# Kernel tuning notes

Hardware: AMD Instinct MI355X
Metric: run time of the kernel (lower is better)

Reference implementation:

```python
import jax, jax.numpy as jnp
import numpy as np

D_MODEL = 1024
N_HEADS = 16
HEAD_DIM = D_MODEL // N_HEADS


def setup_inputs() -> dict:
    key = jax.random.key(0)
    k1, k2, k3, k4, k5 = jax.random.split(key, 5)
    s = 0.02
    return {
        "x": jax.random.normal(k1, (2, 2048, D_MODEL), dtype=jnp.float32),
        "w_qkv": jax.random.normal(k2, (D_MODEL, 3 * D_MODEL), dtype=jnp.float32) * s,
        "b_qkv": jax.random.normal(k3, (3 * D_MODEL,), dtype=jnp.float32) * s,
        "w_proj": jax.random.normal(k4, (D_MODEL, D_MODEL), dtype=jnp.float32) * s,
        "b_proj": jax.random.normal(k5, (D_MODEL,), dtype=jnp.float32) * s,
    }


def reference(x, w_qkv, b_qkv, w_proj, b_proj):
    B, T, C = x.shape
    # fused qkv projection: [B,T,3C] -> [3,B,H,T,Dh]
    qkv = x @ w_qkv + b_qkv
    qkv = qkv.reshape(B, T, 3, N_HEADS, HEAD_DIM).transpose(2, 0, 3, 1, 4)
    q, k, v = qkv[0], qkv[1], qkv[2]
    scale = 1.0 / np.sqrt(HEAD_DIM).astype(np.float32)
    att = jnp.einsum("bhtd,bhsd->bhts", q, k) * scale  # [B,H,T,T]
    causal = jnp.triu(jnp.ones((T, T), dtype=bool), k=1)
    att = jnp.where(causal, -jnp.inf, att)
    att = jax.nn.softmax(att, axis=-1)
    # dropout is identity in eval / p=0
    out = jnp.einsum("bhts,bhsd->bhtd", att, v)  # [B,H,T,Dh]
    out = out.transpose(0, 2, 1, 3).reshape(B, T, C)
    return out @ w_proj + b_proj
```

## Files before the change

### kernel.cpp

```cpp
#include <hip/hip_runtime.h>
#include <hip/hip_bf16.h>
#include <stdint.h>

#define MROWS 4096
#define DMODEL 1024
#define NQKV 3072
#define TSEQ 2048

typedef __attribute__((ext_vector_type(8))) short short8;
typedef __attribute__((ext_vector_type(4))) short short4v;
typedef __attribute__((ext_vector_type(4))) float floatx4;
typedef unsigned short ushort_t;

#define TILE_ELEMS 4608
#define BH_TILE_STRIDE 147456

#define QSCALE 0.1803368801111204f

static __device__ __forceinline__ unsigned short f2bf(float f) {
    union { float f; unsigned u; } v; v.f = f;
    unsigned r = v.u + 0x7fff + ((v.u >> 16) & 1);
    return (unsigned short)(r >> 16);
}


static __device__ __forceinline__ floatx4 mfma16(short4v a, short4v b, floatx4 c) {
#if defined(__HIP_DEVICE_COMPILE__)
#if __has_builtin(__builtin_amdgcn_mfma_f32_16x16x16bf16_1k)
    return __builtin_amdgcn_mfma_f32_16x16x16bf16_1k(a, b, c, 0, 0, 0);
#else
#error "mfma 16x16x16 bf16 builtin unavailable on device"
#endif
#else
    return c;
#endif
}

static __device__ __forceinline__ unsigned pk2bf(float a, float b) {
    unsigned ua = __float_as_uint(a) + 0x8000u;
    unsigned ub = __float_as_uint(b) + 0x8000u;
#if defined(__HIP_DEVICE_COMPILE__) && __has_builtin(__builtin_amdgcn_perm)
    return __builtin_amdgcn_perm(ub, ua, 0x07060302u);
#else
    return (ua >> 16) | (ub & 0xFFFF0000u);
#endif
}

static __device__ __forceinline__ unsigned cvtpk(float a, float b) {
#if defined(__HIP_DEVICE_COMPILE__)
    unsigned r;
    asm("v_cvt_pk_bf16_f32 %0, %1, %2" : "=v"(r) : "v"(a), "v"(b));
    return r;
#else
    return pk2bf(a, b);
#endif
}

static __device__ __forceinline__ float exp2_fast(float x) {
#if defined(__HIP_DEVICE_COMPILE__) && __has_builtin(__builtin_amdgcn_exp2f)
    return __builtin_amdgcn_exp2f(x);
#else
    return exp2f(x);
#endif
}

static __device__ __forceinline__ void glds16(const void* g, void* l) {
    __builtin_amdgcn_global_load_lds(
        (const __attribute__((address_space(1))) void*)g,
        (__attribute__((address_space(3))) void*)l, 16, 0, 0);
}

__global__ void cast_f32_bf16(const float* __restrict__ in,
                              ushort_t* __restrict__ out, int n) {
    int i = (blockIdx.x * blockDim.x + threadIdx.x) * 4;
    if (i < n) {
        float4 f = *(const float4*)(in + i);
        ushort4 o;
        o.x = f2bf(f.x); o.y = f2bf(f.y); o.z = f2bf(f.z); o.w = f2bf(f.w);
        *(ushort4*)(out + i) = o;
    }
}

__global__ void transpose_cast(const float* __restrict__ in,
                               ushort_t* __restrict__ out, int R, int C) {
    __shared__ float tile[32][33];
    int c0 = blockIdx.x * 32, r0 = blockIdx.y * 32;
    int tx = threadIdx.x & 31, ty = threadIdx.x >> 5;
    for (int i = 0; i < 4; i++) {
        int r = ty + i * 8;
        tile[r][tx] = in[(size_t)(r0 + r) * C + c0 + tx];
    }
    __syncthreads();
    for (int i = 0; i < 4; i++) {
        int r = ty + i * 8;
        out[(size_t)(c0 + r) * R + r0 + tx] = f2bf(tile[tx][r]);
    }
}

__global__ void transpose_v(const ushort_t* __restrict__ in,
                            ushort_t* __restrict__ out) {
    __shared__ ushort_t T[64][72];
    int tile = blockIdx.x, bh = blockIdx.y;
    int tid = threadIdx.x;
    int row = tid >> 2, q4 = tid & 3;
    const ushort_t* ip = in + ((size_t)bh * TSEQ + tile * 64) * 64;
#pragma unroll
    for (int p = 0; p < 2; p++) {
        int c = q4 * 16 + p * 8;
        *(uint4*)(&T[row][c]) = *(const uint4*)(ip + (size_t)row * 64 + c);
    }
    __syncthreads();
    ushort_t* op = out + (size_t)bh * BH_TILE_STRIDE + (size_t)tile * TILE_ELEMS;
#pragma unroll
    for (int p = 0; p < 2; p++) {
        int cbase = q4 * 16 + p * 8;
        ushort_t tmp[8];
#pragma unroll
        for (int e = 0; e < 8; e++) {
            int cp = cbase + e;
            int Q = cp >> 4, SB = (cp >> 2) & 3, J = cp & 3;
            int s = SB * 16 + Q * 4 + J;
            tmp[e] = T[s][row];
        }
        *(uint4*)(op + (size_t)row * 72 + cbase) = *(uint4*)tmp;
    }
}

template <int EPI, int MFRAG, int PERXCD>
__global__ __launch_bounds__(256, 3)
void gemm_glds(const ushort_t* __restrict__ A,
               const ushort_t* __restrict__ Bt,
               const float* __restrict__ bias,
               void* __restrict__ out0, void* __restrict__ out1, void* __restrict__ out2,
               int M, int N, int K) {
    __shared__ ushort_t As[MFRAG * 32 * 32];
    __shared__ ushort_t Bs[128 * 32];
    int tid = threadIdx.x;
    int wave = tid >> 6, lane = tid & 63;
    int quad = lane >> 4, l16 = lane & 15;
    int id = blockIdx.x;
    int xcd = id & 7, sidx = id >> 3;
    int m_idx = xcd * PERXCD + (sidx & (PERXCD - 1));
    int n_idx = sidx / PERXCD;
    int m0 = m_idx * (MFRAG * 32), n0 = n_idx * 128;
    int wm = (wave & 1) * (MFRAG * 16), wn = (wave >> 1) * 64;

    const floatx4 zero = {0.f, 0.f, 0.f, 0.f};
    floatx4 acc[MFRAG][4];
#pragma unroll
    for (int i = 0; i < MFRAG; i++)
#pragma unroll
        for (int j = 0; j < 4; j++) acc[i][j] = zero;

    int srow = tid >> 2, sc = tid & 3;
    const ushort_t* ag = A  + (size_t)(m0 + srow) * K + sc * 8;
    const ushort_t* bg = Bt + (size_t)(n0 + srow) * K + sc * 8;
    ushort_t* asw = As + wave * 512;
    ushort_t* bsw = Bs + wave * 512;

    for (int k0 = 0; k0 < K; k0 += 32) {
        glds16(ag + k0, asw);
        if (MFRAG == 4) glds16(ag + (size_t)64 * K + k0, asw + 2048);
        glds16(bg + k0, bsw);
        glds16(bg + (size_t)64 * K + k0, bsw + 2048);
        __syncthreads();
        short8 af[MFRAG], bf[4];
#pragma unroll
        for (int i = 0; i < MFRAG; i++)
            af[i] = *(const short8*)(As + (wm + i * 16 + l16) * 32 + quad * 8);
#pragma unroll
        for (int j = 0; j < 4; j++)
            bf[j] = *(const short8*)(Bs + (wn + j * 16 + l16) * 32 + quad * 8);
#pragma unroll
        for (int i = 0; i < MFRAG; i++)
#pragma unroll
            for (int j = 0; j < 4; j++)
                acc[i][j] = __builtin_amdgcn_mfma_f32_16x16x32_bf16(
                    af[i], bf[j], acc[i][j], 0, 0, 0);
        __syncthreads();
    }

    int sec = n0 >> 10;
    ushort_t* dst = (ushort_t*)(sec == 0 ? out0 : (sec == 1 ? out1 : out2));
#pragma unroll
    for (int i = 0; i < MFRAG; i++) {
        int row = m0 + wm + i * 16 + quad * 4;
#pragma unroll
        for (int j = 0; j < 4; j++) {
            int col = n0 + wn + j * 16 + l16;
            float bvs = bias[col];
#pragma unroll
            for (int r = 0; r < 4; r++) {
                float v = acc[i][j][r] + bvs;
                int rowr = row + r;
                if (EPI == 0) {
                    ((float*)out0)[(size_t)rowr * N + col] = v;
                } else {
                    int b = rowr >> 11, t = rowr & 2047;
                    int within = col & 1023, h = within >> 6, d = within & 63;
                    size_t bh = (size_t)(b * 16 + h);
                    if (sec == 0)
                        dst[(bh * 2048 + t) * 64 + d] = f2bf(v * QSCALE);
                    else if (sec == 1)
                        dst[bh * BH_TILE_STRIDE + (size_t)(t >> 6) * TILE_ELEMS
                            + (size_t)(t & 63) * 72 + d] = f2bf(v);
                    else
                        dst[(bh * 2048 + t) * 64 + d] = f2bf(v);
                }
            }
        }
    }
}

__global__ __launch_bounds__(256, 4)
void attn_kernel(const ushort_t* __restrict__ Qb,
                 const ushort_t* __restrict__ Kt,
                 const ushort_t* __restrict__ Vt,
                 ushort_t* __restrict__ outb) {
    __shared__ ushort_t Ks[2][64 * 72];
    __shared__ ushort_t Vs[2][64 * 72];
    int tid = threadIdx.x;
    int wave = tid >> 6, lane = tid & 63;
    int quad = lane >> 4, l16 = lane & 15;
    int id = blockIdx.x;
    int g = id >> 3;
    int bh = (id & 7) * 4 + (g >> 5);
    int qt = 31 - (g & 31);
    int b = bh >> 4, h = bh & 15;
    const ushort_t* qh = Qb + (size_t)bh * TSEQ * 64;
    const ushort_t* kh = Kt + (size_t)bh * BH_TILE_STRIDE;
    const ushort_t* vh = Vt + (size_t)bh * BH_TILE_STRIDE;
    const floatx4 zero = {0.f, 0.f, 0.f, 0.f};
    const short4v ones = {(short)0x3F80, (short)0x3F80, (short)0x3F80, (short)0x3F80};
    int lo8 = lane * 8;

    int q0 = qt * 64;
    int nsteps = qt + 1;

    int qrow = q0 + wave * 16 + l16;
    short8 qf0 = *(const short8*)(qh + (size_t)qrow * 64 + quad * 8);
    short8 qf1 = *(const short8*)(qh + (size_t)qrow * 64 + 32 + quad * 8);

    floatx4 Oacc[4];
#pragma unroll
    for (int j = 0; j < 4; j++) Oacc[j] = zero;
    floatx4 lacc = zero;

#pragma unroll
    for (int c = 0; c < 3; c++) {
        int cc = wave + 4 * c;
        if (cc < 9) {
            glds16(kh + cc * 512 + lo8, &Ks[0][cc * 512]);
            glds16(vh + cc * 512 + lo8, &Vs[0][cc * 512]);
        }
    }

    for (int step = 0; step < nsteps; step++) {
        int cur = step & 1;
        __syncthreads();
        if (step + 1 < nsteps) {
            const ushort_t* kt = kh + (size_t)(step + 1) * TILE_ELEMS;
            const ushort_t* vt = vh + (size_t)(step + 1) * TILE_ELEMS;
#pragma unroll
            for (int c = 0; c < 3; c++) {
                int cc = wave + 4 * c;
                if (cc < 9) {
                    glds16(kt + cc * 512 + lo8, &Ks[cur ^ 1][cc * 512]);
                    glds16(vt + cc * 512 + lo8, &Vs[cur ^ 1][cc * 512]);
                }
            }
        }
        const ushort_t* ks = &Ks[cur][0];
        const ushort_t* vs = &Vs[cur][0];

        floatx4 S[4];
        __builtin_amdgcn_s_setprio(1);
#pragma unroll
        for (int sb = 0; sb < 4; sb++) {
            short8 kf0 = *(const short8*)(ks + (sb * 16 + l16) * 72 + quad * 8);
            short8 kf1 = *(const short8*)(ks + (sb * 16 + l16) * 72 + 32 + quad * 8);
            floatx4 s = zero;
            s = __builtin_amdgcn_mfma_f32_16x16x32_bf16(kf0, qf0, s, 0, 0, 0);
            s = __builtin_amdgcn_mfma_f32_16x16x32_bf16(kf1, qf1, s, 0, 0, 0);
            S[sb] = s;
        }
        __builtin_amdgcn_s_setprio(0);
        if (step == nsteps - 1) {
            int ql = wave * 16 + l16;
#pragma unroll
            for (int sb = 0; sb < 4; sb++)
#pragma unroll
                for (int r = 0; r < 4; r++)
                    if (sb * 16 + quad * 4 + r > ql) S[sb][r] = -1e30f;
        }
#pragma unroll
        for (int sb = 0; sb < 4; sb++)
#pragma unroll
            for (int r = 0; r < 4; r++)
                S[sb][r] = exp2_fast(S[sb][r]);

        short4v pf[4];
#pragma unroll
        for (int sb = 0; sb < 4; sb++) {
            union { unsigned u[2]; short4v v; } pk;
            pk.u[0] = cvtpk(S[sb][0], S[sb][1]);
            pk.u[1] = cvtpk(S[sb][2], S[sb][3]);
            pf[sb] = pk.v;
        }
        __builtin_amdgcn_s_setprio(1);
        lacc = mfma16(ones, pf[0], lacc);
        lacc = mfma16(ones, pf[1], lacc);
        lacc = mfma16(ones, pf[2], lacc);
        lacc = mfma16(ones, pf[3], lacc);
#pragma unroll
        for (int jd = 0; jd < 4; jd++) {
            const ushort_t* vrow = vs + (jd * 16 + l16) * 72 + quad * 16;
            short8 vA = *(const short8*)(vrow);
            short8 vB = *(const short8*)(vrow + 8);
            short4v v0 = __builtin_shufflevector(vA, vA, 0, 1, 2, 3);
            short4v v1 = __builtin_shufflevector(vA, vA, 4, 5, 6, 7);
            short4v v2 = __builtin_shufflevector(vB, vB, 0, 1, 2, 3);
            short4v v3 = __builtin_shufflevector(vB, vB, 4, 5, 6, 7);
            Oacc[jd] = mfma16(v0, pf[0], Oacc[jd]);
            Oacc[jd] = mfma16(v1, pf[1], Oacc[jd]);
            Oacc[jd] = mfma16(v2, pf[2], Oacc[jd]);
            Oacc[jd] = mfma16(v3, pf[3], Oacc[jd]);
        }
        __builtin_amdgcn_s_setprio(0);
    }
    {
        float rl = 1.0f / lacc[0];
        int row = b * TSEQ + q0 + wave * 16 + l16;
#pragma unroll
        for (int jd = 0; jd < 4; jd++) {
            int col = h * 64 + jd * 16 + quad * 4;
            ushort4 o;
            o.x = f2bf(Oacc[jd][0] * rl);
            o.y = f2bf(Oacc[jd][1] * rl);
            o.z = f2bf(Oacc[jd][2] * rl);
            o.w = f2bf(Oacc[jd][3] * rl);
            *(ushort4*)(outb + (size_t)row * DMODEL + col) = o;
        }
    }
}

extern "C" void kernel_launch(void* const* d_in, const int* in_sizes, int n_in,
                              void* d_out, int out_size, void* d_ws, size_t ws_size,
                              hipStream_t stream) {
    const float* x      = (const float*)d_in[0];
    const float* w_qkv  = (const float*)d_in[1];
    const float* b_qkv  = (const float*)d_in[2];
    const float* w_proj = (const float*)d_in[3];
    const float* b_proj = (const float*)d_in[4];
    float* out = (float*)d_out;
    char* ws = (char*)d_ws;

    ushort_t* xb     = (ushort_t*)(ws);
    ushort_t* Vt     = (ushort_t*)(ws);
    ushort_t* wqkvT  = (ushort_t*)(ws + 8388608);
    ushort_t* wprojT = (ushort_t*)(ws + 10485760);
    ushort_t* Qb     = (ushort_t*)(ws + 14680064);
    ushort_t* Kt     = (ushort_t*)(ws + 23068672);
    ushort_t* Vb     = (ushort_t*)(ws + 32505856);
    ushort_t* attnb  = Vb;

    cast_f32_bf16<<<4096, 256, 0, stream>>>(x, xb, MROWS * DMODEL);
    transpose_cast<<<dim3(NQKV / 32, DMODEL / 32), 256, 0, stream>>>(w_qkv, wqkvT, DMODEL, NQKV);

    gemm_glds<1, 4, 4><<<768, 256, 0, stream>>>(
        xb, wqkvT, b_qkv, Qb, Kt, Vb, MROWS, NQKV, DMODEL);

    transpose_v<<<dim3(32, 32), 256, 0, stream>>>(Vb, Vt);
    transpose_cast<<<dim3(DMODEL / 32, DMODEL / 32), 256, 0, stream>>>(w_proj, wprojT, DMODEL, DMODEL);

    attn_kernel<<<dim3(1024), 256, 0, stream>>>(Qb, Kt, Vt, attnb);

    gemm_glds<0, 2, 8><<<512, 256, 0, stream>>>(
        attnb, wprojT, b_proj, out, nullptr, nullptr, MROWS, DMODEL, DMODEL);
}
```

Measured before the change: 195.4 us.

## Balance causal attention work by splitting long query tiles across blocks

Replaces the one-block-per-query-tile attention kernel with a balanced split. Each block either pairs a short query tile with the first half of a long tile's KV range, or handles the second half of a long tile. For long tiles, unnormalized partial outputs and row sums go to fp32 workspace and are merged by a new combine kernel. A paired-tile fallback kernel, which takes the row sum from a shuffle reduction instead of an MFMA, is used when the workspace is too small. This trades an extra launch and fp32 partial traffic for even per-block work in place of the triangular imbalance.

```diff
diff --git a/kernel.cpp b/kernel.cpp
--- a/kernel.cpp
+++ b/kernel.cpp
@@ -213,7 +213,184 @@
 }
 
 __global__ __launch_bounds__(256, 4)
-void attn_kernel(const ushort_t* __restrict__ Qb,
+void attn_split(const ushort_t* __restrict__ Qb,
+                const ushort_t* __restrict__ Kt,
+                const ushort_t* __restrict__ Vt,
+                ushort_t* __restrict__ outb,
+                float* __restrict__ PO_a, float* __restrict__ PO_b,
+                float* __restrict__ Pl_a, float* __restrict__ Pl_b) {
+    __shared__ ushort_t Ks[2][64 * 72];
+    __shared__ ushort_t Vs[2][64 * 72];
+    int tid = threadIdx.x;
+    int wave = tid >> 6, lane = tid & 63;
+    int quad = lane >> 4, l16 = lane & 15;
+    int id = blockIdx.x;
+    int g = id >> 3;
+    int bh = (id & 7) * 4 + (g >> 5);
+    int rem = g & 31;
+    int p = rem >> 1, sub = rem & 1;
+    int b = bh >> 4, h = bh & 15;
+    const ushort_t* qh = Qb + (size_t)bh * TSEQ * 64;
+    const ushort_t* kh = Kt + (size_t)bh * BH_TILE_STRIDE;
+    const ushort_t* vh = Vt + (size_t)bh * BH_TILE_STRIDE;
+    const floatx4 zero = {0.f, 0.f, 0.f, 0.f};
+    const short4v ones = {(short)0x3F80, (short)0x3F80, (short)0x3F80, (short)0x3F80};
+    int lo8 = lane * 8;
+
+    int nseg = sub ? 1 : 2;
+    for (int seg = 0; seg < nseg; seg++) {
+        int qt, k0, cnt, mode;
+        if (sub)           { qt = 31 - p; k0 = 16 - p; cnt = 16;     mode = 2; }
+        else if (seg == 0) { qt = p;      k0 = 0;      cnt = p + 1;  mode = 0; }
+        else               { qt = 31 - p; k0 = 0;      cnt = 16 - p; mode = 1; }
+
+        int qrow = qt * 64 + wave * 16 + l16;
+        short8 qf0 = *(const short8*)(qh + (size_t)qrow * 64 + quad * 8);
+        short8 qf1 = *(const short8*)(qh + (size_t)qrow * 64 + 32 + quad * 8);
+
+        floatx4 Oacc[4];
+#pragma unroll
+        for (int j = 0; j < 4; j++) Oacc[j] = zero;
+        floatx4 lacc = zero;
+
+        __syncthreads();
+        {
+            const ushort_t* kt0 = kh + (size_t)k0 * TILE_ELEMS;
+            const ushort_t* vt0 = vh + (size_t)k0 * TILE_ELEMS;
+#pragma unroll
+            for (int c = 0; c < 3; c++) {
+                int cc = wave + 4 * c;
+                if (cc < 9) {
+                    glds16(kt0 + cc * 512 + lo8, &Ks[0][cc * 512]);
+                    glds16(vt0 + cc * 512 + lo8, &Vs[0][cc * 512]);
+                }
+            }
+        }
+
+        for (int step = 0; step < cnt; step++) {
+            int cur = step & 1;
+            __syncthreads();
+            if (step + 1 < cnt) {
+                const ushort_t* kt = kh + (size_t)(k0 + step + 1) * TILE_ELEMS;
+                const ushort_t* vt = vh + (size_t)(k0 + step + 1) * TILE_ELEMS;
+#pragma unroll
+                for (int c = 0; c < 3; c++) {
+                    int cc = wave + 4 * c;
+                    if (cc < 9) {
+                        glds16(kt + cc * 512 + lo8, &Ks[cur ^ 1][cc * 512]);
+                        glds16(vt + cc * 512 + lo8, &Vs[cur ^ 1][cc * 512]);
+                    }
+                }
+            }
+            const ushort_t* ks = &Ks[cur][0];
+            const ushort_t* vs = &Vs[cur][0];
+
+            floatx4 S[4];
+            __builtin_amdgcn_s_setprio(1);
+#pragma unroll
+            for (int sb = 0; sb < 4; sb++) {
+                short8 kf0 = *(const short8*)(ks + (sb * 16 + l16) * 72 + quad * 8);
+                short8 kf1 = *(const short8*)(ks + (sb * 16 + l16) * 72 + 32 + quad * 8);
+                floatx4 s = zero;
+                s = __builtin_amdgcn_mfma_f32_16x16x32_bf16(kf0, qf0, s, 0, 0, 0);
+                s = __builtin_amdgcn_mfma_f32_16x16x32_bf16(kf1, qf1, s, 0, 0, 0);
+                S[sb] = s;
+            }
+            __builtin_amdgcn_s_setprio(0);
+            if (k0 + step == qt) {
+                int ql = wave * 16 + l16;
+#pragma unroll
+                for (int sb = 0; sb < 4; sb++)
+#pragma unroll
+                    for (int r = 0; r < 4; r++)
+                        if (sb * 16 + quad * 4 + r > ql) S[sb][r] = -1e30f;
+            }
+#pragma unroll
+            for (int sb = 0; sb < 4; sb++)
+#pragma unroll
+                for (int r = 0; r < 4; r++)
+                    S[sb][r] = exp2_fast(S[sb][r]);
+
+            short4v pf[4];
+#pragma unroll
+            for (int sb = 0; sb < 4; sb++) {
+                union { unsigned u[2]; short4v v; } pk;
+                pk.u[0] = cvtpk(S[sb][0], S[sb][1]);
+                pk.u[1] = cvtpk(S[sb][2], S[sb][3]);
+                pf[sb] = pk.v;
+            }
+            __builtin_amdgcn_s_setprio(1);
+            lacc = mfma16(ones, pf[0], lacc);
+            lacc = mfma16(ones, pf[1], lacc);
+            lacc = mfma16(ones, pf[2], lacc);
+            lacc = mfma16(ones, pf[3], lacc);
+#pragma unroll
+            for (int jd = 0; jd < 4; jd++) {
+                const ushort_t* vrow = vs + (jd * 16 + l16) * 72 + quad * 16;
+                short8 vA = *(const short8*)(vrow);
+                short8 vB = *(const short8*)(vrow + 8);
+                short4v v0 = __builtin_shufflevector(vA, vA, 0, 1, 2, 3);
+                short4v v1 = __builtin_shufflevector(vA, vA, 4, 5, 6, 7);
+                short4v v2 = __builtin_shufflevector(vB, vB, 0, 1, 2, 3);
+                short4v v3 = __builtin_shufflevector(vB, vB, 4, 5, 6, 7);
+                Oacc[jd] = mfma16(v0, pf[0], Oacc[jd]);
+                Oacc[jd] = mfma16(v1, pf[1], Oacc[jd]);
+                Oacc[jd] = mfma16(v2, pf[2], Oacc[jd]);
+                Oacc[jd] = mfma16(v3, pf[3], Oacc[jd]);
+            }
+            __builtin_amdgcn_s_setprio(0);
+        }
+
+        if (mode == 0) {
+            float rl = 1.0f / lacc[0];
+            int row = b * TSEQ + qt * 64 + wave * 16 + l16;
+#pragma unroll
+            for (int jd = 0; jd < 4; jd++) {
+                int col = h * 64 + jd * 16 + quad * 4;
+                ushort4 o;
+                o.x = f2bf(Oacc[jd][0] * rl);
+                o.y = f2bf(Oacc[jd][1] * rl);
+                o.z = f2bf(Oacc[jd][2] * rl);
+                o.w = f2bf(Oacc[jd][3] * rl);
+                *(ushort4*)(outb + (size_t)row * DMODEL + col) = o;
+            }
+        } else {
+            float* PO = (mode == 1) ? PO_a : PO_b;
+            float* Pl = (mode == 1) ? Pl_a : Pl_b;
+            int prow = (qt - 16) * 64 + wave * 16 + l16;
+            size_t rbase = ((size_t)bh * 1024 + prow) * 64;
+#pragma unroll
+            for (int jd = 0; jd < 4; jd++)
+                *(floatx4*)(PO + rbase + jd * 16 + quad * 4) = Oacc[jd];
+            if (quad == 0) Pl[(size_t)bh * 1024 + prow] = lacc[0];
+        }
+    }
+}
+
+__global__ void attn_combine(const float* __restrict__ PO_a,
+                             const float* __restrict__ PO_b,
+                             const float* __restrict__ Pl_a,
+                             const float* __restrict__ Pl_b,
+                             ushort_t* __restrict__ outb) {
+    int i = blockIdx.x * 256 + threadIdx.x;
+    int row = i >> 4;
+    int c4 = (i & 15) * 4;
+    float rl = 1.0f / (Pl_a[row] + Pl_b[row]);
+    floatx4 a = *(const floatx4*)(PO_a + (size_t)row * 64 + c4);
+    floatx4 c = *(const floatx4*)(PO_b + (size_t)row * 64 + c4);
+    int bh = row >> 10, prow = row & 1023;
+    int b = bh >> 4, h = bh & 15;
+    int orow = b * TSEQ + 1024 + prow;
+    ushort4 o;
+    o.x = f2bf((a[0] + c[0]) * rl);
+    o.y = f2bf((a[1] + c[1]) * rl);
+    o.z = f2bf((a[2] + c[2]) * rl);
+    o.w = f2bf((a[3] + c[3]) * rl);
+    *(ushort4*)(outb + (size_t)orow * DMODEL + h * 64 + c4) = o;
+}
+
+__global__ __launch_bounds__(256, 1)
+void attn_paired(const ushort_t* __restrict__ Qb,
                  const ushort_t* __restrict__ Kt,
                  const ushort_t* __restrict__ Vt,
                  ushort_t* __restrict__ outb) {
@@ -222,125 +399,126 @@
     int tid = threadIdx.x;
     int wave = tid >> 6, lane = tid & 63;
     int quad = lane >> 4, l16 = lane & 15;
-    int id = blockIdx.x;
-    int g = id >> 3;
-    int bh = (id & 7) * 4 + (g >> 5);
-    int qt = 31 - (g & 31);
+    int pair = blockIdx.x;
+    int bh = blockIdx.y;
     int b = bh >> 4, h = bh & 15;
     const ushort_t* qh = Qb + (size_t)bh * TSEQ * 64;
     const ushort_t* kh = Kt + (size_t)bh * BH_TILE_STRIDE;
     const ushort_t* vh = Vt + (size_t)bh * BH_TILE_STRIDE;
     const floatx4 zero = {0.f, 0.f, 0.f, 0.f};
-    const short4v ones = {(short)0x3F80, (short)0x3F80, (short)0x3F80, (short)0x3F80};
     int lo8 = lane * 8;
 
-    int q0 = qt * 64;
-    int nsteps = qt + 1;
-
-    int qrow = q0 + wave * 16 + l16;
-    short8 qf0 = *(const short8*)(qh + (size_t)qrow * 64 + quad * 8);
-    short8 qf1 = *(const short8*)(qh + (size_t)qrow * 64 + 32 + quad * 8);
-
-    floatx4 Oacc[4];
-#pragma unroll
-    for (int j = 0; j < 4; j++) Oacc[j] = zero;
-    floatx4 lacc = zero;
-
-#pragma unroll
-    for (int c = 0; c < 3; c++) {
-        int cc = wave + 4 * c;
-        if (cc < 9) {
-            glds16(kh + cc * 512 + lo8, &Ks[0][cc * 512]);
-            glds16(vh + cc * 512 + lo8, &Vs[0][cc * 512]);
-        }
-    }
-
-    for (int step = 0; step < nsteps; step++) {
-        int cur = step & 1;
+    for (int half = 0; half < 2; half++) {
+        int qt = half ? (31 - pair) : pair;
+        int q0 = qt * 64;
+        int nsteps = qt + 1;
+
+        int qrow = q0 + wave * 16 + l16;
+        short8 qf0 = *(const short8*)(qh + (size_t)qrow * 64 + quad * 8);
+        short8 qf1 = *(const short8*)(qh + (size_t)qrow * 64 + 32 + quad * 8);
+
+        floatx4 Oacc[4];
+#pragma unroll
+        for (int j = 0; j < 4; j++) Oacc[j] = zero;
+        float lsum = 0.f;
+
+#pragma unroll
+        for (int c = 0; c < 3; c++) {
+            int cc = wave + 4 * c;
+            if (cc < 9) {
+                glds16(kh + cc * 512 + lo8, &Ks[0][cc * 512]);
+                glds16(vh + cc * 512 + lo8, &Vs[0][cc * 512]);
+            }
+        }
+
+        for (int step = 0; step < nsteps; step++) {
+            int cur = step & 1;
+            __syncthreads();
+            if (step + 1 < nsteps) {
+                const ushort_t* kt = kh + (size_t)(step + 1) * TILE_ELEMS;
+                const ushort_t* vt = vh + (size_t)(step + 1) * TILE_ELEMS;
+#pragma unroll
+                for (int c = 0; c < 3; c++) {
+                    int cc = wave + 4 * c;
+                    if (cc < 9) {
+                        glds16(kt + cc * 512 + lo8, &Ks[cur ^ 1][cc * 512]);
+                        glds16(vt + cc * 512 + lo8, &Vs[cur ^ 1][cc * 512]);
+                    }
+                }
+            }
+            const ushort_t* ks = &Ks[cur][0];
+            const ushort_t* vs = &Vs[cur][0];
+
+            floatx4 S[4];
+#pragma unroll
+            for (int sb = 0; sb < 4; sb++) {
+                short8 kf0 = *(const short8*)(ks + (sb * 16 + l16) * 72 + quad * 8);
+                short8 kf1 = *(const short8*)(ks + (sb * 16 + l16) * 72 + 32 + quad * 8);
+                floatx4 s = zero;
+                s = __builtin_amdgcn_mfma_f32_16x16x32_bf16(kf0, qf0, s, 0, 0, 0);
+                s = __builtin_amdgcn_mfma_f32_16x16x32_bf16(kf1, qf1, s, 0, 0, 0);
+                S[sb] = s;
+            }
+            if (step == nsteps - 1) {
+                int ql = wave * 16 + l16;
+#pragma unroll
+                for (int sb = 0; sb < 4; sb++)
+#pragma unroll
+                    for (int r = 0; r < 4; r++)
+                        if (sb * 16 + quad * 4 + r > ql) S[sb][r] = -1e30f;
+            }
+            float sum = 0.f;
+#pragma unroll
+            for (int sb = 0; sb < 4; sb++)
+#pragma unroll
+                for (int r = 0; r < 4; r++) {
+                    float p = exp2_fast(S[sb][r]);
+                    S[sb][r] = p;
+                    sum += p;
+                }
+            lsum += sum;
+
+            short4v pf[4];
+#pragma unroll
+            for (int sb = 0; sb < 4; sb++) {
+                union { unsigned u[2]; short4v v; } pk;
+                pk.u[0] = pk2bf(S[sb][0], S[sb][1]);
+                pk.u[1] = pk2bf(S[sb][2], S[sb][3]);
+                pf[sb] = pk.v;
+            }
+#pragma unroll
+            for (int jd = 0; jd < 4; jd++) {
+                const ushort_t* vrow = vs + (jd * 16 + l16) * 72 + quad * 16;
+                short8 vA = *(const short8*)(vrow);
+                short8 vB = *(const short8*)(vrow + 8);
+                short4v v0 = __builtin_shufflevector(vA, vA, 0, 1, 2, 3);
+                short4v v1 = __builtin_shufflevector(vA, vA, 4, 5, 6, 7);
+                short4v v2 = __builtin_shufflevector(vB, vB, 0, 1, 2, 3);
+                short4v v3 = __builtin_shufflevector(vB, vB, 4, 5, 6, 7);
+                Oacc[jd] = mfma16(v0, pf[0], Oacc[jd]);
+                Oacc[jd] = mfma16(v1, pf[1], Oacc[jd]);
+                Oacc[jd] = mfma16(v2, pf[2], Oacc[jd]);
+                Oacc[jd] = mfma16(v3, pf[3], Oacc[jd]);
+            }
+        }
+        {
+            float l = lsum;
+            l += __shfl_xor(l, 16);
+            l += __shfl_xor(l, 32);
+            float rl = 1.0f / l;
+            int row = b * TSEQ + q0 + wave * 16 + l16;
+#pragma unroll
+            for (int jd = 0; jd < 4; jd++) {
+                int col = h * 64 + jd * 16 + quad * 4;
+                ushort4 o;
+                o.x = f2bf(Oacc[jd][0] * rl);
+                o.y = f2bf(Oacc[jd][1] * rl);
+                o.z = f2bf(Oacc[jd][2] * rl);
+                o.w = f2bf(Oacc[jd][3] * rl);
+                *(ushort4*)(outb + (size_t)row * DMODEL + col) = o;
+            }
+        }
         __syncthreads();
-        if (step + 1 < nsteps) {
-            const ushort_t* kt = kh + (size_t)(step + 1) * TILE_ELEMS;
-            const ushort_t* vt = vh + (size_t)(step + 1) * TILE_ELEMS;
-#pragma unroll
-            for (int c = 0; c < 3; c++) {
-                int cc = wave + 4 * c;
-                if (cc < 9) {
-                    glds16(kt + cc * 512 + lo8, &Ks[cur ^ 1][cc * 512]);
-                    glds16(vt + cc * 512 + lo8, &Vs[cur ^ 1][cc * 512]);
-                }
-            }
-        }
-        const ushort_t* ks = &Ks[cur][0];
-        const ushort_t* vs = &Vs[cur][0];
-
-        floatx4 S[4];
-        __builtin_amdgcn_s_setprio(1);
-#pragma unroll
-        for (int sb = 0; sb < 4; sb++) {
-            short8 kf0 = *(const short8*)(ks + (sb * 16 + l16) * 72 + quad * 8);
-            short8 kf1 = *(const short8*)(ks + (sb * 16 + l16) * 72 + 32 + quad * 8);
-            floatx4 s = zero;
-            s = __builtin_amdgcn_mfma_f32_16x16x32_bf16(kf0, qf0, s, 0, 0, 0);
-            s = __builtin_amdgcn_mfma_f32_16x16x32_bf16(kf1, qf1, s, 0, 0, 0);
-            S[sb] = s;
-        }
-        __builtin_amdgcn_s_setprio(0);
-        if (step == nsteps - 1) {
-            int ql = wave * 16 + l16;
-#pragma unroll
-            for (int sb = 0; sb < 4; sb++)
-#pragma unroll
-                for (int r = 0; r < 4; r++)
-                    if (sb * 16 + quad * 4 + r > ql) S[sb][r] = -1e30f;
-        }
-#pragma unroll
-        for (int sb = 0; sb < 4; sb++)
-#pragma unroll
-            for (int r = 0; r < 4; r++)
-                S[sb][r] = exp2_fast(S[sb][r]);
-
-        short4v pf[4];
-#pragma unroll
-        for (int sb = 0; sb < 4; sb++) {
-            union { unsigned u[2]; short4v v; } pk;
-            pk.u[0] = cvtpk(S[sb][0], S[sb][1]);
-            pk.u[1] = cvtpk(S[sb][2], S[sb][3]);
-            pf[sb] = pk.v;
-        }
-        __builtin_amdgcn_s_setprio(1);
-        lacc = mfma16(ones, pf[0], lacc);
-        lacc = mfma16(ones, pf[1], lacc);
-        lacc = mfma16(ones, pf[2], lacc);
-        lacc = mfma16(ones, pf[3], lacc);
-#pragma unroll
-        for (int jd = 0; jd < 4; jd++) {
-            const ushort_t* vrow = vs + (jd * 16 + l16) * 72 + quad * 16;
-            short8 vA = *(const short8*)(vrow);
-            short8 vB = *(const short8*)(vrow + 8);
-            short4v v0 = __builtin_shufflevector(vA, vA, 0, 1, 2, 3);
-            short4v v1 = __builtin_shufflevector(vA, vA, 4, 5, 6, 7);
-            short4v v2 = __builtin_shufflevector(vB, vB, 0, 1, 2, 3);
-            short4v v3 = __builtin_shufflevector(vB, vB, 4, 5, 6, 7);
-            Oacc[jd] = mfma16(v0, pf[0], Oacc[jd]);
-            Oacc[jd] = mfma16(v1, pf[1], Oacc[jd]);
-            Oacc[jd] = mfma16(v2, pf[2], Oacc[jd]);
-            Oacc[jd] = mfma16(v3, pf[3], Oacc[jd]);
-        }
-        __builtin_amdgcn_s_setprio(0);
-    }
-    {
-        float rl = 1.0f / lacc[0];
-        int row = b * TSEQ + q0 + wave * 16 + l16;
-#pragma unroll
-        for (int jd = 0; jd < 4; jd++) {
-            int col = h * 64 + jd * 16 + quad * 4;
-            ushort4 o;
-            o.x = f2bf(Oacc[jd][0] * rl);
-            o.y = f2bf(Oacc[jd][1] * rl);
-            o.z = f2bf(Oacc[jd][2] * rl);
-            o.w = f2bf(Oacc[jd][3] * rl);
-            *(ushort4*)(outb + (size_t)row * DMODEL + col) = o;
-        }
     }
 }
 
@@ -363,6 +541,11 @@
     ushort_t* Kt     = (ushort_t*)(ws + 23068672);
     ushort_t* Vb     = (ushort_t*)(ws + 32505856);
     ushort_t* attnb  = Vb;
+    float* PO_a = (float*)(ws + 40894464);
+    float* PO_b = (float*)(ws + 49283072);
+    float* Pl_a = (float*)(ws + 57671680);
+    float* Pl_b = (float*)(ws + 57802752);
+    const size_t ws_need = 57933824;
 
     cast_f32_bf16<<<4096, 256, 0, stream>>>(x, xb, MROWS * DMODEL);
     transpose_cast<<<dim3(NQKV / 32, DMODEL / 32), 256, 0, stream>>>(w_qkv, wqkvT, DMODEL, NQKV);
@@ -373,7 +556,13 @@
     transpose_v<<<dim3(32, 32), 256, 0, stream>>>(Vb, Vt);
     transpose_cast<<<dim3(DMODEL / 32, DMODEL / 32), 256, 0, stream>>>(w_proj, wprojT, DMODEL, DMODEL);
 
-    attn_kernel<<<dim3(1024), 256, 0, stream>>>(Qb, Kt, Vt, attnb);
+    if (ws_size >= ws_need) {
+        attn_split<<<dim3(1024), 256, 0, stream>>>(Qb, Kt, Vt, attnb,
+                                                   PO_a, PO_b, Pl_a, Pl_b);
+        attn_combine<<<dim3(2048), 256, 0, stream>>>(PO_a, PO_b, Pl_a, Pl_b, attnb);
+    } else {
+        attn_paired<<<dim3(16, 32), 256, 0, stream>>>(Qb, Kt, Vt, attnb);
+    }
 
     gemm_glds<0, 2, 8><<<512, 256, 0, stream>>>(
         attnb, wprojT, b_proj, out, nullptr, nullptr, MROWS, DMODEL, DMODEL);
```

Measured after the change: 187.6 us. 4.0% less time.
